# Kernel optimization log

Hardware: AMD Instinct MI355X
Metric: run time of the kernel (lower is better)

Reference implementation:

```python
import jax, jax.numpy as jnp
import numpy as np
import math

T, B, D, H, L, C = 2048, 64, 256, 256, 2, 2
HIGHWAY_BIAS = 0.0
# SRU rescale factor for the highway skip term (rescale=True)
SCALE_X = (1.0 + math.exp(HIGHWAY_BIAS * 2)) ** 0.5


def setup_inputs() -> dict:
    key = jax.random.key(0)
    ks = jax.random.split(key, 8)
    s = 1.0 / np.sqrt(D)
    x = jax.random.normal(ks[0], (T, B, D), dtype=jnp.float32)
    # per-layer SRU weights: W [D, 3H] -> (x_tilde, f, r); bias [2H] -> (b_f, b_r)
    W1 = jax.random.uniform(ks[1], (D, 3 * H), jnp.float32, -s, s)
    b1 = jnp.zeros((2 * H,), jnp.float32)
    W2 = jax.random.uniform(ks[2], (H, 3 * H), jnp.float32, -s, s)
    b2 = jnp.zeros((2 * H,), jnp.float32)
    lin_W = jax.random.uniform(ks[3], (H, C), jnp.float32, -s, s)
    lin_b = jnp.zeros((C,), jnp.float32)
    return {"x": x, "W1": W1, "b1": b1, "W2": W2, "b2": b2,
            "lin_W": lin_W, "lin_b": lin_b}


def _sru_layer(x, W, b):
    # x: [T, B, D]; W: [D, 3H]; b: [2H]. Skip term uses raw x (D == H).
    U = jnp.einsum('tbd,dk->tbk', x, W)           # [T, B, 3H]
    x_tilde, f_raw, r_raw = jnp.split(U, 3, axis=-1)
    b_f, b_r = jnp.split(b, 2)
    f = jax.nn.sigmoid(f_raw + b_f + HIGHWAY_BIAS)  # [T, B, H]
    r = jax.nn.sigmoid(r_raw + b_r)                 # [T, B, H]

    def step(c, inp):
        f_t, xt_t = inp
        c = f_t * c + (1.0 - f_t) * xt_t
        return c, c

    c0 = jnp.zeros(x.shape[1:], x.dtype)            # [B, H]
    _, cs = jax.lax.scan(step, c0, (f, x_tilde))    # cs: [T, B, H]
    h = r * cs + (1.0 - r) * (x * SCALE_X)          # highway skip (rescaled)
    return h


def reference(x, W1, b1, W2, b2, lin_W, lin_b):
    h1 = _sru_layer(x, W1, b1)
    h2 = _sru_layer(h1, W2, b2)
    last = h2[-1]                                   # [B, H] (last timestep)
    # Dropout in eval mode = identity (deterministic reference)
    return last @ lin_W + lin_b                     # [B, C]
```

## Files before the change

kernel.cpp:

```cpp
#include <hip/hip_runtime.h>
#include <hip/hip_bf16.h>
#include <stdint.h>

#define T_LEN 2048
#define B_SZ  64
#define H_SZ  256
#define NH3   768
#define M_SZ  (T_LEN * B_SZ)
#define NC    64
#define TC    32
#define SCALE_X_F 1.41421356237309515f

typedef __attribute__((ext_vector_type(8))) short short8;
typedef __attribute__((ext_vector_type(4))) float f32x4;

__device__ __forceinline__ float sigmoidf_(float z) {
    return 1.0f / (1.0f + __expf(-z));
}
__device__ __forceinline__ unsigned short f2bf(float f) {
    unsigned u = __float_as_uint(f);
    return (unsigned short)((u + 0x7FFFu + ((u >> 16) & 1u)) >> 16);
}
__device__ __forceinline__ float bf2f(unsigned short s) {
    return __uint_as_float(((unsigned)s) << 16);
}

__global__ void k_convert_x(const float* __restrict__ x, unsigned short* __restrict__ xb) {
    int i = blockIdx.x * blockDim.x + threadIdx.x;
    const float4* in = (const float4*)x;
    float4 a = in[i * 2];
    float4 b = in[i * 2 + 1];
    short8 o;
    o[0] = (short)f2bf(a.x); o[1] = (short)f2bf(a.y);
    o[2] = (short)f2bf(a.z); o[3] = (short)f2bf(a.w);
    o[4] = (short)f2bf(b.x); o[5] = (short)f2bf(b.y);
    o[6] = (short)f2bf(b.z); o[7] = (short)f2bf(b.w);
    *(short8*)&xb[(size_t)i * 8] = o;
}

__global__ void k_prep_w(const float* __restrict__ W, unsigned short* __restrict__ Wt) {
    int i = blockIdx.x * 256 + threadIdx.x;
    int n = i >> 8, k = i & 255;
    Wt[i] = f2bf(W[(size_t)k * NH3 + n]);
}

template <int NT, int CS, int TPB>
__global__ void __launch_bounds__(256, 2)
k_gemm(const unsigned short* __restrict__ A,
       const unsigned short* __restrict__ Bt,
       unsigned short* __restrict__ C) {
    __shared__ alignas(16) unsigned short lds[2][16384];

    int orig = blockIdx.x;
    int xcd = orig & 7, b_in = orig >> 3;
    const int MT_PER_XCD = TPB * 64 / NT;

    int tid = threadIdx.x;
    int w = tid >> 6, l = tid & 63;
    int r16 = l & 15, kg = l >> 4;
    int wr = w >> 1, wc = w & 1;
    int scol = ((l & 7) ^ (l >> 3)) * 8;
    int srow = (l >> 3);

    auto tile_mb = [&](int s) {
        int tau = s * 64 + b_in;
        return (xcd * MT_PER_XCD + tau / NT) * 128;
    };
    auto tile_nb = [&](int s) {
        int tau = s * 64 + b_in;
        return (tau % NT) * 128;
    };

    auto stage = [&](int mb, int nb, int kt, int b) {
        #pragma unroll
        for (int p = 0; p < 4; ++p) {
            int row = w * 32 + p * 8 + srow;
            const unsigned short* ga = A  + (size_t)(mb + row) * 256 + kt * 64 + scol;
            const unsigned short* gb = Bt + (size_t)(nb + row) * 256 + kt * 64 + scol;
            __builtin_amdgcn_global_load_lds(
                (const __attribute__((address_space(1))) void*)ga,
                (__attribute__((address_space(3))) void*)&lds[b][(w * 4 + p) * 512], 16, 0, 0);
            __builtin_amdgcn_global_load_lds(
                (const __attribute__((address_space(1))) void*)gb,
                (__attribute__((address_space(3))) void*)&lds[b][8192 + (w * 4 + p) * 512], 16, 0, 0);
        }
    };

    stage(tile_mb(0), tile_nb(0), 0, 0);

    #pragma unroll 1
    for (int s = 0; s < TPB; ++s) {
        int mbase = tile_mb(s), nbase = tile_nb(s);
        int sn = (s + 1 < TPB) ? s + 1 : s;
        int mb_n = tile_mb(sn), nb_n = tile_nb(sn);

        f32x4 acc[4][4];
        #pragma unroll
        for (int m = 0; m < 4; ++m)
            #pragma unroll
            for (int n = 0; n < 4; ++n) {
                f32x4 z = {0.f, 0.f, 0.f, 0.f};
                acc[m][n] = z;
            }

        #pragma unroll
        for (int kt = 0; kt < 4; ++kt) {
            if (kt < 3) stage(mbase, nbase, kt + 1, (kt + 1) & 1);
            else        stage(mb_n, nb_n, 0, 0);

            asm volatile("s_waitcnt vmcnt(8)" ::: "memory");
            __builtin_amdgcn_s_barrier();
            asm volatile("" ::: "memory");

            const unsigned short* As = &lds[kt & 1][0];
            const unsigned short* Bs = &lds[kt & 1][8192];
            short8 af[4][2], bfv[4][2];
            #pragma unroll
            for (int m = 0; m < 4; ++m) {
                int arow = wr * 64 + m * 16 + r16;
                int sw = (arow & 7) << 3;
                #pragma unroll
                for (int kk = 0; kk < 2; ++kk)
                    af[m][kk] = *(const short8*)&As[arow * 64 + ((kk * 32 + kg * 8) ^ sw)];
            }
            #pragma unroll
            for (int n = 0; n < 4; ++n) {
                int brow = wc * 64 + n * 16 + r16;
                int sw = (brow & 7) << 3;
                #pragma unroll
                for (int kk = 0; kk < 2; ++kk)
                    bfv[n][kk] = *(const short8*)&Bs[brow * 64 + ((kk * 32 + kg * 8) ^ sw)];
            }

            __builtin_amdgcn_s_setprio(1);
            #pragma unroll
            for (int m = 0; m < 4; ++m)
                #pragma unroll
                for (int n = 0; n < 4; ++n)
                    #pragma unroll
                    for (int kk = 0; kk < 2; ++kk)
                        acc[m][n] = __builtin_amdgcn_mfma_f32_16x16x32_bf16(
                            af[m][kk], bfv[n][kk], acc[m][n], 0, 0, 0);
            __builtin_amdgcn_s_setprio(0);

            asm volatile("" ::: "memory");
            __builtin_amdgcn_s_barrier();
            asm volatile("" ::: "memory");
        }

        unsigned short* ep = &lds[1][0];
        #pragma unroll
        for (int m = 0; m < 4; ++m)
            #pragma unroll
            for (int n = 0; n < 4; ++n) {
                int col = wc * 64 + n * 16 + r16;
                #pragma unroll
                for (int r = 0; r < 4; ++r) {
                    int row = wr * 64 + m * 16 + kg * 4 + r;
                    ep[row * 128 + (col ^ ((row & 7) << 3))] = f2bf(acc[m][n][r]);
                }
            }
        asm volatile("s_waitcnt lgkmcnt(0)" ::: "memory");
        __builtin_amdgcn_s_barrier();
        asm volatile("" ::: "memory");
        #pragma unroll
        for (int st = 0; st < 8; ++st) {
            int slot = st * 256 + tid;
            int row = slot >> 4, seg = slot & 15;
            short8 v = *(const short8*)&ep[row * 128 + ((seg * 8) ^ ((row & 7) << 3))];
            *(short8*)&C[(size_t)(mbase + row) * CS + nbase + seg * 8] = v;
        }
        asm volatile("s_waitcnt lgkmcnt(0)" ::: "memory");
        __builtin_amdgcn_s_barrier();
        asm volatile("" ::: "memory");
    }
}

__global__ void k_passA(const unsigned short* __restrict__ U, const float* __restrict__ bias,
                        float* __restrict__ P, float* __restrict__ S, int stride) {
    int ci = blockIdx.x >> 6;
    int b  = blockIdx.x & 63;
    int h  = threadIdx.x;
    float bfv = bias[h];
    size_t base = ((size_t)(ci * TC) * B_SZ + b) * stride + h;
    float c = 0.f, pr = 1.f;
    #pragma unroll 4
    for (int t = 0; t < TC; ++t) {
        float xt = bf2f(U[base]);
        float fr = bf2f(U[base + 256]);
        float f = sigmoidf_(fr + bfv);
        c = f * c + (1.f - f) * xt;
        pr *= f;
        base += (size_t)B_SZ * stride;
    }
    int o = blockIdx.x * 256 + h;
    P[o] = pr;
    S[o] = c;
}

__global__ void k_passB(const float* __restrict__ P, const float* __restrict__ S,
                        float* __restrict__ cin) {
    int b = blockIdx.x, h = threadIdx.x;
    int idx = b * 256 + h;
    float c = 0.f;
    #pragma unroll 8
    for (int ci = 0; ci < NC; ++ci) {
        cin[ci * 16384 + idx] = c;
        c = P[ci * 16384 + idx] * c + S[ci * 16384 + idx];
    }
    cin[NC * 16384 + idx] = c;
}

__global__ void k_passC(const unsigned short* __restrict__ U, const float* __restrict__ bias,
                        const unsigned short* __restrict__ xb, const float* __restrict__ cin,
                        unsigned short* __restrict__ hout) {
    int ci = blockIdx.x >> 6, b = blockIdx.x & 63, h = threadIdx.x;
    float bfv = bias[h], brv = bias[256 + h];
    float c = cin[blockIdx.x * 256 + h];
    size_t base  = ((size_t)(ci * TC) * B_SZ + b) * NH3 + h;
    size_t xbase = ((size_t)(ci * TC) * B_SZ + b) * H_SZ + h;
    #pragma unroll 4
    for (int t = 0; t < TC; ++t) {
        float xt = bf2f(U[base]);
        float fr = bf2f(U[base + 256]);
        float rr = bf2f(U[base + 512]);
        float f = sigmoidf_(fr + bfv);
        float r = sigmoidf_(rr + brv);
        c = f * c + (1.f - f) * xt;
        float xv = bf2f(xb[xbase]);
        hout[xbase] = f2bf(r * c + (1.f - r) * xv * SCALE_X_F);
        base  += (size_t)B_SZ * NH3;
        xbase += (size_t)B_SZ * H_SZ;
    }
}

__global__ void k_final(const unsigned short* __restrict__ h1, const float* __restrict__ cin,
                        const float* __restrict__ W2, const float* __restrict__ b2,
                        const float* __restrict__ lw, const float* __restrict__ lb,
                        float* __restrict__ out) {
    int b = blockIdx.x, h = threadIdx.x;
    __shared__ float hrow[256];
    size_t hb = ((size_t)(T_LEN - 1) * B_SZ + b) * H_SZ;
    hrow[h] = bf2f(h1[hb + h]);
    __syncthreads();
    float rr = 0.f;
    #pragma unroll 8
    for (int k = 0; k < 256; ++k)
        rr += hrow[k] * W2[(size_t)k * NH3 + 512 + h];
    float r = sigmoidf_(rr + b2[256 + h]);
    float c = cin[NC * 16384 + b * 256 + h];
    float hv = r * c + (1.f - r) * hrow[h] * SCALE_X_F;
    float p0 = hv * lw[h * 2];
    float p1 = hv * lw[h * 2 + 1];
    #pragma unroll
    for (int off = 32; off; off >>= 1) {
        p0 += __shfl_down(p0, off);
        p1 += __shfl_down(p1, off);
    }
    __shared__ float s0[4], s1[4];
    int wid = h >> 6, lane = h & 63;
    if (lane == 0) { s0[wid] = p0; s1[wid] = p1; }
    __syncthreads();
    if (h == 0) {
        out[b * 2]     = s0[0] + s0[1] + s0[2] + s0[3] + lb[0];
        out[b * 2 + 1] = s1[0] + s1[1] + s1[2] + s1[3] + lb[1];
    }
}

extern "C" void kernel_launch(void* const* d_in, const int* in_sizes, int n_in,
                              void* d_out, int out_size, void* d_ws, size_t ws_size,
                              hipStream_t stream) {
    const float* x   = (const float*)d_in[0];
    const float* W1  = (const float*)d_in[1];
    const float* b1  = (const float*)d_in[2];
    const float* W2  = (const float*)d_in[3];
    const float* b2  = (const float*)d_in[4];
    const float* lw  = (const float*)d_in[5];
    const float* lb  = (const float*)d_in[6];
    float* out = (float*)d_out;

    char* ws = (char*)d_ws;
    unsigned short* U   = (unsigned short*)ws;
    unsigned short* xb  = (unsigned short*)(ws + 201326592);
    unsigned short* h1  = (unsigned short*)(ws + 268435456);
    unsigned short* Wt1 = (unsigned short*)(ws + 335544320);
    unsigned short* Wt2 = (unsigned short*)(ws + 335937536);
    float* Pbuf = (float*)(ws + 336330752);
    float* Sbuf = (float*)(ws + 340525056);
    float* cin  = (float*)(ws + 344719360);

    k_convert_x<<<16384, 256, 0, stream>>>(x, xb);
    k_prep_w<<<768, 256, 0, stream>>>(W1, Wt1);
    k_prep_w<<<512, 256, 0, stream>>>(W2, Wt2);

    k_gemm<6, NH3, 12><<<512, 256, 0, stream>>>(xb, Wt1, U);
    k_passA<<<4096, 256, 0, stream>>>(U, b1, Pbuf, Sbuf, NH3);
    k_passB<<<64, 256, 0, stream>>>(Pbuf, Sbuf, cin);
    k_passC<<<4096, 256, 0, stream>>>(U, b1, xb, cin, h1);

    k_gemm<4, 512, 8><<<512, 256, 0, stream>>>(h1, Wt2, U);
    k_passA<<<4096, 256, 0, stream>>>(U, b2, Pbuf, Sbuf, 512);
    k_passB<<<64, 256, 0, stream>>>(Pbuf, Sbuf, cin);
    k_final<<<64, 256, 0, stream>>>(h1, cin, W2, b2, lw, lb, out);
}
```

Before: 359.0 us.

## Pre-pack x and W1 into MFMA fragment layout for an LDS-free layer-1 GEMM

The x conversion kernel now also writes a copy of bf16 x in a fragment-major layout, stored in the h1 buffer. W1 is packed the same way. A new GEMM kernel reads MFMA operands straight from global memory with no LDS staging for inputs and uses LDS only for a swizzled epilogue store. The persistent k_gemm for layer 1 is replaced by a 6144-block launch. This removes LDS traffic and barriers in the main loop, at the cost of writing x twice and depending on cache reuse of the global operand loads.

```diff
diff --git a/kernel.cpp b/kernel.cpp
--- a/kernel.cpp
+++ b/kernel.cpp
@@ -25,23 +25,114 @@
     return __uint_as_float(((unsigned)s) << 16);
 }
 
-__global__ void k_convert_x(const float* __restrict__ x, unsigned short* __restrict__ xb) {
-    int i = blockIdx.x * blockDim.x + threadIdx.x;
-    const float4* in = (const float4*)x;
-    float4 a = in[i * 2];
-    float4 b = in[i * 2 + 1];
-    short8 o;
-    o[0] = (short)f2bf(a.x); o[1] = (short)f2bf(a.y);
-    o[2] = (short)f2bf(a.z); o[3] = (short)f2bf(a.w);
-    o[4] = (short)f2bf(b.x); o[5] = (short)f2bf(b.y);
-    o[6] = (short)f2bf(b.z); o[7] = (short)f2bf(b.w);
-    *(short8*)&xb[(size_t)i * 8] = o;
+__global__ void k_convert_x(const float* __restrict__ x,
+                            unsigned short* __restrict__ xb,
+                            unsigned short* __restrict__ xfm) {
+    int gid = blockIdx.x * 256 + threadIdx.x;
+    int rm = gid >> 2, kg = gid & 3;
+    const float* xp = x + (size_t)rm * 256 + kg * 8;
+    unsigned short* rowp = xb + (size_t)rm * 256 + kg * 8;
+    unsigned short* fmp  = xfm + (size_t)(rm >> 4) * 4096 + kg * 128 + (rm & 15) * 8;
+    #pragma unroll
+    for (int kt = 0; kt < 8; ++kt) {
+        float4 a = *(const float4*)(xp + kt * 32);
+        float4 b = *(const float4*)(xp + kt * 32 + 4);
+        short8 o;
+        o[0] = (short)f2bf(a.x); o[1] = (short)f2bf(a.y);
+        o[2] = (short)f2bf(a.z); o[3] = (short)f2bf(a.w);
+        o[4] = (short)f2bf(b.x); o[5] = (short)f2bf(b.y);
+        o[6] = (short)f2bf(b.z); o[7] = (short)f2bf(b.w);
+        *(short8*)(rowp + kt * 32)  = o;
+        *(short8*)(fmp + kt * 512) = o;
+    }
 }
 
 __global__ void k_prep_w(const float* __restrict__ W, unsigned short* __restrict__ Wt) {
     int i = blockIdx.x * 256 + threadIdx.x;
     int n = i >> 8, k = i & 255;
     Wt[i] = f2bf(W[(size_t)k * NH3 + n]);
+}
+
+__global__ void k_prep_w_fm(const float* __restrict__ W, unsigned short* __restrict__ Bfm) {
+    int gid = blockIdx.x * 256 + threadIdx.x;
+    int n = gid >> 2, kg = gid & 3;
+    unsigned short* fmp = Bfm + (size_t)(n >> 4) * 4096 + kg * 128 + (n & 15) * 8;
+    #pragma unroll
+    for (int kt = 0; kt < 8; ++kt) {
+        short8 o;
+        #pragma unroll
+        for (int e = 0; e < 8; ++e)
+            o[e] = (short)f2bf(W[(size_t)(kt * 32 + kg * 8 + e) * NH3 + n]);
+        *(short8*)(fmp + kt * 512) = o;
+    }
+}
+
+template <int NT, int CS>
+__global__ void __launch_bounds__(256, 3)
+k_gemm_fm(const unsigned short* __restrict__ Afm,
+          const unsigned short* __restrict__ Bfm,
+          unsigned short* __restrict__ C) {
+    __shared__ alignas(16) unsigned short ep[128 * 128];
+
+    const int cpx = (1024 * NT) / 8;
+    int orig = blockIdx.x;
+    int wgid = (orig & 7) * cpx + (orig >> 3);
+    int mt = wgid / NT, nt = wgid % NT;
+
+    int tid = threadIdx.x;
+    int w = tid >> 6, l = tid & 63;
+    int r16 = l & 15, kg = l >> 4;
+    int wr = w >> 1, wc = w & 1;
+
+    const unsigned short* ab = Afm + (size_t)(mt * 64 + wr * 32) * 512 + l * 8;
+    const unsigned short* bb = Bfm + (size_t)(nt * 64 + wc * 32) * 512 + l * 8;
+
+    f32x4 acc[4][4];
+    #pragma unroll
+    for (int m = 0; m < 4; ++m)
+        #pragma unroll
+        for (int n = 0; n < 4; ++n) {
+            f32x4 z = {0.f, 0.f, 0.f, 0.f};
+            acc[m][n] = z;
+        }
+
+    #pragma unroll
+    for (int kt = 0; kt < 8; ++kt) {
+        short8 af[4], bf[4];
+        #pragma unroll
+        for (int m = 0; m < 4; ++m)
+            af[m] = *(const short8*)(ab + (size_t)(m * 8 + kt) * 512);
+        #pragma unroll
+        for (int n = 0; n < 4; ++n)
+            bf[n] = *(const short8*)(bb + (size_t)(n * 8 + kt) * 512);
+        #pragma unroll
+        for (int m = 0; m < 4; ++m)
+            #pragma unroll
+            for (int n = 0; n < 4; ++n)
+                acc[m][n] = __builtin_amdgcn_mfma_f32_16x16x32_bf16(
+                    af[m], bf[n], acc[m][n], 0, 0, 0);
+    }
+
+    int mbase = mt * 128, nbase = nt * 128;
+    #pragma unroll
+    for (int m = 0; m < 4; ++m)
+        #pragma unroll
+        for (int n = 0; n < 4; ++n) {
+            int col = wc * 64 + n * 16 + r16;
+            #pragma unroll
+            for (int r = 0; r < 4; ++r) {
+                int row = wr * 64 + m * 16 + kg * 4 + r;
+                ep[row * 128 + (col ^ ((row & 7) << 3))] = f2bf(acc[m][n][r]);
+            }
+        }
+    __syncthreads();
+    #pragma unroll
+    for (int s = 0; s < 8; ++s) {
+        int slot = s * 256 + tid;
+        int row = slot >> 4, seg = slot & 15;
+        short8 v = *(const short8*)&ep[row * 128 + ((seg * 8) ^ ((row & 7) << 3))];
+        *(short8*)&C[(size_t)(mbase + row) * CS + nbase + seg * 8] = v;
+    }
 }
 
 template <int NT, int CS, int TPB>
@@ -289,11 +380,13 @@
     float* Sbuf = (float*)(ws + 340525056);
     float* cin  = (float*)(ws + 344719360);
 
-    k_convert_x<<<16384, 256, 0, stream>>>(x, xb);
-    k_prep_w<<<768, 256, 0, stream>>>(W1, Wt1);
+    unsigned short* xfm = h1;
+
+    k_convert_x<<<2048, 256, 0, stream>>>(x, xb, xfm);
+    k_prep_w_fm<<<12, 256, 0, stream>>>(W1, Wt1);
     k_prep_w<<<512, 256, 0, stream>>>(W2, Wt2);
 
-    k_gemm<6, NH3, 12><<<512, 256, 0, stream>>>(xb, Wt1, U);
+    k_gemm_fm<6, NH3><<<6144, 256, 0, stream>>>(xfm, Wt1, U);
     k_passA<<<4096, 256, 0, stream>>>(U, b1, Pbuf, Sbuf, NH3);
     k_passB<<<64, 256, 0, stream>>>(Pbuf, Sbuf, cin);
     k_passC<<<4096, 256, 0, stream>>>(U, b1, xb, cin, h1);
```

After: 415.6 us. 1.16x slower.
